# Performance work log

Hardware: AMD Instinct MI355X
Metric: run time of the kernel (lower is better)

Reference implementation:

```python
import jax, jax.numpy as jnp
import numpy as np

H, W = 512, 512  # spatial shape from init_kwargs
N_PTS = 200000
C_IN, C_OUT, K, PAD = 64, 128, 3, 1


def setup_inputs() -> dict:
    key = jax.random.key(0)
    k1, k2, k3, k4 = jax.random.split(key, 4)
    batch_size = 4
    features = jax.random.normal(k1, (N_PTS, C_IN), dtype=jnp.float32)
    b = jax.random.randint(k2, (N_PTS, 1), 0, batch_size, dtype=jnp.int32)
    yx = jax.random.randint(k3, (N_PTS, 2), 0, H, dtype=jnp.int32)  # y,x in [0, 512)
    coors = jnp.concatenate([b, yx], axis=1)  # [N, 3] = (batch, y, x)
    # spconv conv weight, expressed OIHW for lax.conv
    weight = jax.random.normal(k4, (C_OUT, C_IN, K, K), dtype=jnp.float32) * (1.0 / np.sqrt(C_IN * K * K))
    return {"features": features, "coors": coors, "batch_size": batch_size, "weight": weight}


def reference(features, coors, batch_size, weight):
    # SparseConvTensor -> densify: scatter-add point features onto the [B, C, H, W] grid
    # (add is faithful to spconv's gather-GEMM-scatter handling of duplicate coords).
    dense = jnp.zeros((batch_size, features.shape[1], H, W), dtype=features.dtype)
    dense = dense.at[coors[:, 0], :, coors[:, 1], coors[:, 2]].add(features)
    # SparseConv2d(stride=1, padding=1, bias=None) == dense conv on the densified grid;
    # inactive output sites are exactly zero, so this matches the densified sparse output.
    out = jax.lax.conv_general_dilated(
        dense, weight,
        window_strides=(1, 1),
        padding=[(PAD, PAD), (PAD, PAD)],
        dimension_numbers=("NCHW", "OIHW", "NCHW"),
    )
    return out  # [B, C_out, H, W]
```

## Files before the change

kernel.cpp:

```cpp
#include <hip/hip_runtime.h>
#include <stdint.h>

#define HH 512
#define WW 512
#define CIN 64
#define COUT 128
#define NB 4
#define HP 514
#define WP 520
#define STRIP 128
#define SCOLS 136
#define NCHUNK 17
#define SLAB_B (SCOLS * CIN * 2)

typedef __bf16 bf16x8 __attribute__((ext_vector_type(8)));
typedef float f32x4 __attribute__((ext_vector_type(4)));
typedef const __attribute__((address_space(1))) uint32_t guint_t;
typedef __attribute__((address_space(3))) uint32_t luint_t;

__device__ __forceinline__ unsigned short f2bf(float f) {
    union { float f; uint32_t u; } v; v.f = f;
    uint32_t u = v.u;
    u += 0x7fffu + ((u >> 16) & 1u);
    return (unsigned short)(u >> 16);
}
__device__ __forceinline__ float bf2f(uint32_t u) {
    union { uint32_t u; float f; } v; v.u = u << 16;
    return v.f;
}

__global__ void zero_kernel(float4* __restrict__ p, long n4) {
    long i = (long)blockIdx.x * 256 + threadIdx.x;
    const long stride = (long)gridDim.x * 256;
    const float4 z = make_float4(0.f, 0.f, 0.f, 0.f);
    for (; i < n4; i += stride) p[i] = z;
}

__global__ void wt_transform(const float* __restrict__ w, unsigned short* __restrict__ wt2) {
    int tid = blockIdx.x * 256 + threadIdx.x;
    if (tid >= COUT * 576) return;
    int co = tid / 576;
    int k  = tid - co * 576;
    int off = k >> 6;
    int ci  = k & 63;
    int ky = off / 3;
    int kx = off - ky * 3;
    float val = w[((co * CIN + ci) * 3 + ky) * 3 + kx];
    wt2[(size_t)(k >> 3) * (COUT * 8) + co * 8 + (k & 7)] = f2bf(val);
}

__global__ void scatter_kernel(const float* __restrict__ feat,
                               const int* __restrict__ coors,
                               uint32_t* __restrict__ dpad, int npts) {
    int t = blockIdx.x * 256 + threadIdx.x;
    int p = t >> 5;
    int c2 = t & 31;
    if (p >= npts) return;
    int b = coors[p * 3 + 0];
    int y = coors[p * 3 + 1];
    int x = coors[p * 3 + 2];
    uint32_t* wp = dpad + (((size_t)b * HP + (y + 1)) * WP + (x + 1)) * (CIN / 2) + c2;
    float ax = feat[(size_t)p * CIN + c2 * 2];
    float ay = feat[(size_t)p * CIN + c2 * 2 + 1];
    uint32_t old = *wp, assumed;
    do {
        assumed = old;
        uint32_t nv = (uint32_t)f2bf(bf2f(assumed & 0xffffu) + ax)
                    | ((uint32_t)f2bf(bf2f(assumed >> 16) + ay) << 16);
        old = atomicCAS(wp, assumed, nv);
    } while (old != assumed);
}

__global__ __launch_bounds__(256, 3) void conv_kernel(
        const __bf16* __restrict__ dpad,
        const __bf16* __restrict__ wt2,
        float* __restrict__ out) {
    __shared__ __align__(16) __bf16 lds[3 * SCOLS * CIN];

    const int bid = blockIdx.x;
    const int xs = bid & 3;
    const int y  = (bid >> 2) & 511;
    const int b  = bid >> 11;
    const int x0 = xs * STRIP;
    const int tid = threadIdx.x;
    const int wave = tid >> 6;
    const int lane = tid & 63;
    const int lhi = lane >> 4;
    const int llo = lane & 15;
    const int site_base = (wave & 1) * 64;
    const int co_base   = (wave >> 1) * 64;

    const char* gbase = (const char*)dpad;
    #pragma unroll
    for (int r = 0; r < 3; ++r) {
        const char* rowp = gbase + (((size_t)b * HP + (y + r)) * WP + x0) * (CIN * 2);
        char* lslab = ((char*)lds) + r * SLAB_B;
        #pragma unroll
        for (int i = 0; i < 5; ++i) {
            int c = wave + i * 4;
            if (c < NCHUNK) {
                int P = c * 1024 + lane * 16;
                int L = P ^ (((P >> 7) & 7) << 4);
                __builtin_amdgcn_global_load_lds(
                    (guint_t*)(rowp + L), (luint_t*)(lslab + c * 1024), 16, 0, 0);
            }
        }
    }
    __syncthreads();

    f32x4 acc[4][4];
    #pragma unroll
    for (int mt = 0; mt < 4; ++mt)
        #pragma unroll
        for (int nt = 0; nt < 4; ++nt)
            acc[mt][nt] = (f32x4){0.f, 0.f, 0.f, 0.f};

    #pragma unroll
    for (int off = 0; off < 9; ++off) {
        const int ky = off / 3;
        const int kx = off - ky * 3;
        const char* slab = (const char*)lds + ky * SLAB_B;
        #pragma unroll
        for (int ch = 0; ch < 2; ++ch) {
            bf16x8 a[4];
            #pragma unroll
            for (int mt = 0; mt < 4; ++mt) {
                int col = site_base + mt * 16 + llo + kx;
                int eb = (ch * 64 + lhi * 16) ^ ((col & 7) << 4);
                a[mt] = *reinterpret_cast<const bf16x8*>(slab + col * 128 + eb);
            }
            const __bf16* bb = wt2 + (size_t)(off * 8 + ch * 4 + lhi) * (COUT * 8);
            #pragma unroll
            for (int nt = 0; nt < 4; ++nt) {
                bf16x8 bw = *reinterpret_cast<const bf16x8*>(
                    &bb[(co_base + nt * 16 + llo) * 8]);
                #pragma unroll
                for (int mt = 0; mt < 4; ++mt)
                    acc[mt][nt] = __builtin_amdgcn_mfma_f32_16x16x32_bf16(
                        a[mt], bw, acc[mt][nt], 0, 0, 0);
            }
        }
    }

    #pragma unroll
    for (int nt = 0; nt < 4; ++nt) {
        int co = co_base + nt * 16 + llo;
        float* orow = out + ((size_t)(b * COUT + co) * HH + y) * WW
                          + x0 + site_base + lhi * 4;
        #pragma unroll
        for (int mt = 0; mt < 4; ++mt)
            __builtin_nontemporal_store(acc[mt][nt],
                reinterpret_cast<f32x4*>(&orow[mt * 16]));
    }
}

extern "C" void kernel_launch(void* const* d_in, const int* in_sizes, int n_in,
                              void* d_out, int out_size, void* d_ws, size_t ws_size,
                              hipStream_t stream) {
    const float* feat  = (const float*)d_in[0];
    const int*   coors = (const int*)d_in[1];
    const float* w     = (const float*)d_in[3];
    float* out = (float*)d_out;

    const size_t dpad_bytes = (size_t)NB * HP * WP * CIN * 2;
    __bf16* dpad = (__bf16*)d_ws;
    unsigned short* wt2 = (unsigned short*)((char*)d_ws + dpad_bytes);

    const int npts = in_sizes[0] / CIN;

    hipLaunchKernelGGL(zero_kernel, dim3(2048), dim3(256), 0, stream,
                       (float4*)dpad, (long)(dpad_bytes / 16));
    hipLaunchKernelGGL(wt_transform, dim3((COUT * 576 + 255) / 256), dim3(256), 0, stream,
                       w, wt2);
    hipLaunchKernelGGL(scatter_kernel, dim3((npts * 32 + 255) / 256), dim3(256), 0, stream,
                       feat, coors, (uint32_t*)dpad, npts);
    hipLaunchKernelGGL(conv_kernel, dim3(NB * 512 * (WW / STRIP)), dim3(256), 0, stream,
                       dpad, (const __bf16*)wt2, out);
}
```

Before: 265.0 us.

## Double-buffer conv weight loads, fuse zero and weight transform, drop nontemporal stores

The conv kernel now prefetches the weight fragments for the next 3x3 offset into a second register buffer while the MFMAs for the current offset run. The first prefetch is issued before the LDS slab load, so global weight latency is hidden, at the cost of extra VGPRs that may hurt occupancy at launch bounds of 3. The zero-fill and weight-transform kernels are merged into one launch to save a kernel launch. Output stores switch from nontemporal to regular stores.

```diff
diff --git a/kernel.cpp b/kernel.cpp
--- a/kernel.cpp
+++ b/kernel.cpp
@@ -29,24 +29,24 @@
     return v.f;
 }
 
-__global__ void zero_kernel(float4* __restrict__ p, long n4) {
+__global__ void init_kernel(float4* __restrict__ dz, long n4,
+                            const float* __restrict__ w,
+                            unsigned short* __restrict__ wt2) {
     long i = (long)blockIdx.x * 256 + threadIdx.x;
     const long stride = (long)gridDim.x * 256;
     const float4 z = make_float4(0.f, 0.f, 0.f, 0.f);
-    for (; i < n4; i += stride) p[i] = z;
-}
-
-__global__ void wt_transform(const float* __restrict__ w, unsigned short* __restrict__ wt2) {
-    int tid = blockIdx.x * 256 + threadIdx.x;
-    if (tid >= COUT * 576) return;
-    int co = tid / 576;
-    int k  = tid - co * 576;
-    int off = k >> 6;
-    int ci  = k & 63;
-    int ky = off / 3;
-    int kx = off - ky * 3;
-    float val = w[((co * CIN + ci) * 3 + ky) * 3 + kx];
-    wt2[(size_t)(k >> 3) * (COUT * 8) + co * 8 + (k & 7)] = f2bf(val);
+    for (long j = i; j < n4; j += stride) dz[j] = z;
+    int tid = (int)i;
+    if (tid < COUT * 576) {
+        int co = tid / 576;
+        int k  = tid - co * 576;
+        int off = k >> 6;
+        int ci  = k & 63;
+        int ky = off / 3;
+        int kx = off - ky * 3;
+        float val = w[((co * CIN + ci) * 3 + ky) * 3 + kx];
+        wt2[(size_t)(k >> 3) * (COUT * 8) + co * 8 + (k & 7)] = f2bf(val);
+    }
 }
 
 __global__ void scatter_kernel(const float* __restrict__ feat,
@@ -90,6 +90,21 @@
     const int site_base = (wave & 1) * 64;
     const int co_base   = (wave >> 1) * 64;
 
+    auto ldbw = [&](int o9, bf16x8* dst) {
+        #pragma unroll
+        for (int ch = 0; ch < 2; ++ch) {
+            const __bf16* bb = wt2 + (size_t)(o9 * 8 + ch * 4 + lhi) * (COUT * 8);
+            #pragma unroll
+            for (int nt = 0; nt < 4; ++nt)
+                dst[ch * 4 + nt] = *reinterpret_cast<const bf16x8*>(
+                    &bb[(co_base + nt * 16 + llo) * 8]);
+        }
+    };
+
+    bf16x8 bwA[8], bwB[8];
+    ldbw(0, bwA);
+    __builtin_amdgcn_sched_barrier(0);
+
     const char* gbase = (const char*)dpad;
     #pragma unroll
     for (int r = 0; r < 3; ++r) {
@@ -116,10 +131,14 @@
             acc[mt][nt] = (f32x4){0.f, 0.f, 0.f, 0.f};
 
     #pragma unroll
-    for (int off = 0; off < 9; ++off) {
-        const int ky = off / 3;
-        const int kx = off - ky * 3;
+    for (int off9 = 0; off9 < 9; ++off9) {
+        const int ky = off9 / 3;
+        const int kx = off9 - ky * 3;
         const char* slab = (const char*)lds + ky * SLAB_B;
+        bf16x8* curw = (off9 & 1) ? bwB : bwA;
+        bf16x8* nxtw = (off9 & 1) ? bwA : bwB;
+        if (off9 < 8) ldbw(off9 + 1, nxtw);
+        __builtin_amdgcn_sched_barrier(0);
         #pragma unroll
         for (int ch = 0; ch < 2; ++ch) {
             bf16x8 a[4];
@@ -129,15 +148,12 @@
                 int eb = (ch * 64 + lhi * 16) ^ ((col & 7) << 4);
                 a[mt] = *reinterpret_cast<const bf16x8*>(slab + col * 128 + eb);
             }
-            const __bf16* bb = wt2 + (size_t)(off * 8 + ch * 4 + lhi) * (COUT * 8);
             #pragma unroll
             for (int nt = 0; nt < 4; ++nt) {
-                bf16x8 bw = *reinterpret_cast<const bf16x8*>(
-                    &bb[(co_base + nt * 16 + llo) * 8]);
                 #pragma unroll
                 for (int mt = 0; mt < 4; ++mt)
                     acc[mt][nt] = __builtin_amdgcn_mfma_f32_16x16x32_bf16(
-                        a[mt], bw, acc[mt][nt], 0, 0, 0);
+                        a[mt], curw[ch * 4 + nt], acc[mt][nt], 0, 0, 0);
             }
         }
     }
@@ -149,8 +165,7 @@
                           + x0 + site_base + lhi * 4;
         #pragma unroll
         for (int mt = 0; mt < 4; ++mt)
-            __builtin_nontemporal_store(acc[mt][nt],
-                reinterpret_cast<f32x4*>(&orow[mt * 16]));
+            *reinterpret_cast<f32x4*>(&orow[mt * 16]) = acc[mt][nt];
     }
 }
 
@@ -168,10 +183,8 @@
 
     const int npts = in_sizes[0] / CIN;
 
-    hipLaunchKernelGGL(zero_kernel, dim3(2048), dim3(256), 0, stream,
-                       (float4*)dpad, (long)(dpad_bytes / 16));
-    hipLaunchKernelGGL(wt_transform, dim3((COUT * 576 + 255) / 256), dim3(256), 0, stream,
-                       w, wt2);
+    hipLaunchKernelGGL(init_kernel, dim3(2048), dim3(256), 0, stream,
+                       (float4*)dpad, (long)(dpad_bytes / 16), w, wt2);
     hipLaunchKernelGGL(scatter_kernel, dim3((npts * 32 + 255) / 256), dim3(256), 0, stream,
                        feat, coors, (uint32_t*)dpad, npts);
     hipLaunchKernelGGL(conv_kernel, dim3(NB * 512 * (WW / STRIP)), dim3(256), 0, stream,
```

Result: slower. 283.2 us (+6.9%).
